# Kernel tuning notes

Measured on AMD Instinct MI355X. Metric: run time of the kernel, lower is better.

Reference implementation:

```python
import jax, jax.numpy as jnp
import numpy as np

N_NODES = 100000
N_EDGES = 1600000
NUM_GRAPHS = 1024
D_IN = 128
D_HID = 128
D_OUT = 2
LN_EPS = 1e-5


def setup_inputs() -> dict:
    key = jax.random.key(0)
    ks = jax.random.split(key, 10)
    x = jax.random.normal(ks[0], (N_NODES, D_IN), dtype=jnp.float32)
    edge_index = jax.random.randint(ks[1], (2, N_EDGES), 0, N_NODES, dtype=jnp.int64)
    batch = jnp.sort(jax.random.randint(ks[2], (N_NODES,), 0, NUM_GRAPHS, dtype=jnp.int64))
    s = 0.05  # weight scale to keep activations sane
    return {
        "x": x,
        "edge_index": edge_index,
        "batch": batch,
        "W1l": jax.random.normal(ks[3], (D_HID, D_IN), dtype=jnp.float32) * s,
        "b1l": jnp.zeros((D_HID,), dtype=jnp.float32),
        "W1r": jax.random.normal(ks[4], (D_HID, D_IN), dtype=jnp.float32) * s,
        "W2l": jax.random.normal(ks[5], (D_HID, D_HID), dtype=jnp.float32) * s,
        "b2l": jnp.zeros((D_HID,), dtype=jnp.float32),
        "W2r": jax.random.normal(ks[6], (D_HID, D_HID), dtype=jnp.float32) * s,
        "ln_g": jnp.ones((D_HID,), dtype=jnp.float32),
        "ln_b": jnp.zeros((D_HID,), dtype=jnp.float32),
        "Wlin": jax.random.normal(ks[7], (D_OUT, D_HID), dtype=jnp.float32) * s,
        "blin": jnp.zeros((D_OUT,), dtype=jnp.float32),
    }


def _sage_conv(x, src, dst, Wl, bl, Wr):
    # PyG SAGEConv with mean aggregation: lin_l(mean_{j in N(i)} x_j) + lin_r(x_i)
    msg_sum = jax.ops.segment_sum(x[src], dst, num_segments=N_NODES)
    deg = jax.ops.segment_sum(jnp.ones((src.shape[0], 1), x.dtype), dst, num_segments=N_NODES)
    agg = msg_sum / jnp.maximum(deg, 1.0)  # isolated nodes -> 0
    return agg @ Wl.T + bl + x @ Wr.T  # lin_r has no bias (PyG default)


def reference(x, edge_index, batch, W1l, b1l, W1r, W2l, b2l, W2r, ln_g, ln_b, Wlin, blin):
    src, dst = edge_index[0], edge_index[1]
    h = jax.nn.relu(_sage_conv(x, src, dst, W1l, b1l, W1r))
    h = jax.nn.relu(_sage_conv(h, src, dst, W2l, b2l, W2r))
    # global_add_pool over graphs
    g = jax.ops.segment_sum(h, batch, num_segments=NUM_GRAPHS)  # [G, D_HID]
    # LayerNorm over last dim
    mu = jnp.mean(g, axis=-1, keepdims=True)
    var = jnp.var(g, axis=-1, keepdims=True)
    gn = (g - mu) * jax.lax.rsqrt(var + LN_EPS) * ln_g + ln_b
    return gn @ Wlin.T + blin  # [G, D_OUT]
```

## Files before the change

### kernel.cpp

```cpp
#include <hip/hip_runtime.h>
#include <hip/hip_bf16.h>
#include <hip/hip_fp8.h>

#define N_NODES   100000
#define N_EDGES   1600000
#define NUM_GRAPHS 1024
#define D         128
#define LN_EPS    1e-5f
#define NBUCKETS  391
#define CAP       4864
#define CHUNK     4096

typedef __attribute__((ext_vector_type(8))) short short8;
typedef __attribute__((ext_vector_type(4))) float floatx4;
typedef __attribute__((ext_vector_type(2))) float f32x2;

static __device__ __forceinline__ float bf2f(unsigned int u) {
    return __uint_as_float(u << 16);
}
static __device__ __forceinline__ unsigned short f2bf(float f) {
    __hip_bfloat16 h = __float2bfloat16(f);
    return *reinterpret_cast<unsigned short*>(&h);
}
static __device__ __forceinline__ void acc4(f32x2* acc, uint4 v) {
    acc[0] += (f32x2){__uint_as_float(v.x << 16), __uint_as_float(v.x & 0xffff0000u)};
    acc[1] += (f32x2){__uint_as_float(v.y << 16), __uint_as_float(v.y & 0xffff0000u)};
    acc[2] += (f32x2){__uint_as_float(v.z << 16), __uint_as_float(v.z & 0xffff0000u)};
    acc[3] += (f32x2){__uint_as_float(v.w << 16), __uint_as_float(v.w & 0xffff0000u)};
}

#if __has_builtin(__builtin_amdgcn_cvt_pk_f32_fp8)
#define UNPK_FP8(x, w) __builtin_amdgcn_cvt_pk_f32_fp8((x), (w))
#else
static __device__ __forceinline__ f32x2 unpk_fp8_sw(unsigned x, bool w) {
    unsigned s = w ? (x >> 16) : (x & 0xffffu);
    __hip_fp8_e4m3 a, b;
    *reinterpret_cast<unsigned char*>(&a) = (unsigned char)(s & 0xff);
    *reinterpret_cast<unsigned char*>(&b) = (unsigned char)((s >> 8) & 0xff);
    return (f32x2){(float)a, (float)b};
}
#define UNPK_FP8(x, w) unpk_fp8_sw((x), (w))
#endif

#if __has_builtin(__builtin_amdgcn_cvt_pk_fp8_f32)
#define PK_FP8(a, b, old, w) ((unsigned)__builtin_amdgcn_cvt_pk_fp8_f32((a), (b), (int)(old), (w)))
#else
static __device__ __forceinline__ unsigned pk_fp8_sw(float a, float b) {
    __hip_fp8_e4m3 fa = (__hip_fp8_e4m3)a;
    __hip_fp8_e4m3 fb = (__hip_fp8_e4m3)b;
    return (unsigned)*reinterpret_cast<unsigned char*>(&fa) |
           ((unsigned)*reinterpret_cast<unsigned char*>(&fb) << 8);
}
#define PK_FP8(a, b, old, w) ((w) ? ((((unsigned)(old)) & 0xffffu) | (pk_fp8_sw((a),(b)) << 16)) \
                                  : ((((unsigned)(old)) & 0xffff0000u) | pk_fp8_sw((a),(b))))
#endif

__global__ __launch_bounds__(256)
void prep_kernel(const float* __restrict__ x, unsigned short* __restrict__ xbf,
                 unsigned* __restrict__ xf8,
                 const float* __restrict__ W1l, const float* __restrict__ W1r,
                 const float* __restrict__ W2l, const float* __restrict__ W2r,
                 unsigned short* __restrict__ Wc1, unsigned short* __restrict__ Wc2,
                 int* __restrict__ cursor) {
    int i = blockIdx.x * 256 + threadIdx.x;
    float4 v = reinterpret_cast<const float4*>(x)[i];
    ushort4 o;
    o.x = f2bf(v.x); o.y = f2bf(v.y); o.z = f2bf(v.z); o.w = f2bf(v.w);
    reinterpret_cast<ushort4*>(xbf)[i] = o;
    unsigned p = PK_FP8(v.x, v.y, 0u, false);
    p = PK_FP8(v.z, v.w, p, true);
    xf8[i] = p;
    if (blockIdx.x < 256) {
        int layer = i >> 15;
        int rem = i & 32767;
        int c = rem >> 8;
        int k = rem & 255;
        const float* Wl = layer ? W2l : W1l;
        const float* Wr = layer ? W2r : W1r;
        unsigned short* dst = layer ? Wc2 : Wc1;
        float wv = (k < 128) ? Wl[c * 128 + k] : Wr[c * 128 + (k - 128)];
        dst[c * 256 + k] = f2bf(wv);
    }
    if (blockIdx.x == 256) {
        for (int b = threadIdx.x; b < NBUCKETS; b += 256)
            cursor[b] = b * CAP;
    }
}

__global__ __launch_bounds__(256)
void cvt_h1_kernel(const unsigned short* __restrict__ h1, uint2* __restrict__ h1f8) {
    int i = blockIdx.x * 256 + threadIdx.x;
    uint4 v = reinterpret_cast<const uint4*>(h1)[i];
    float c0 = __uint_as_float(v.x << 16), c1 = __uint_as_float(v.x & 0xffff0000u);
    float c2 = __uint_as_float(v.y << 16), c3 = __uint_as_float(v.y & 0xffff0000u);
    float c4 = __uint_as_float(v.z << 16), c5 = __uint_as_float(v.z & 0xffff0000u);
    float c6 = __uint_as_float(v.w << 16), c7 = __uint_as_float(v.w & 0xffff0000u);
    unsigned lo = PK_FP8(c0, c1, 0u, false);
    lo = PK_FP8(c2, c3, lo, true);
    unsigned hi = PK_FP8(c4, c5, 0u, false);
    hi = PK_FP8(c6, c7, hi, true);
    h1f8[i] = make_uint2(lo, hi);
}

__global__ __launch_bounds__(256)
void bin_scatter_kernel(const int* __restrict__ src, const int* __restrict__ dst,
                        int* __restrict__ cursor, unsigned* __restrict__ binned) {
    __shared__ int cnt[NBUCKETS];
    __shared__ int base[NBUCKETS];
    int chunkBase = blockIdx.x * CHUNK;
    for (int i = threadIdx.x; i < NBUCKETS; i += 256) cnt[i] = 0;
    __syncthreads();
    int es[16], ed[16], lofs[16];
    #pragma unroll
    for (int j = 0; j < 16; ++j) {
        int e = chunkBase + j * 256 + threadIdx.x;
        if (e < N_EDGES) {
            es[j] = src[e];
            ed[j] = dst[e];
            lofs[j] = atomicAdd(&cnt[ed[j] >> 8], 1);
        }
    }
    __syncthreads();
    for (int i = threadIdx.x; i < NBUCKETS; i += 256) {
        int c = cnt[i];
        base[i] = c ? atomicAdd(&cursor[i], c) : 0;
    }
    __syncthreads();
    #pragma unroll
    for (int j = 0; j < 16; ++j) {
        int e = chunkBase + j * 256 + threadIdx.x;
        if (e < N_EDGES) {
            int b = ed[j] >> 8;
            int pos = base[b] + lofs[j];
            if (pos < (b + 1) * CAP)
                binned[pos] = ((unsigned)(ed[j] & 255) << 17) | (unsigned)es[j];
        }
    }
}

__global__ __launch_bounds__(256)
void bucket_build_kernel(const unsigned* __restrict__ binned, const int* __restrict__ cursor,
                         int2* __restrict__ row_info, int* __restrict__ src_sorted) {
    __shared__ int scnt[256];
    __shared__ int sscan[256];
    int b = blockIdx.x;
    int t = threadIdx.x;
    int lo = b * CAP;
    int hi = cursor[b];
    int cap_end = lo + CAP;
    if (hi > cap_end) hi = cap_end;
    scnt[t] = 0;
    __syncthreads();
    unsigned rec[19];
    short rnk[19];
    #pragma unroll
    for (int i = 0; i < 19; ++i) {
        int e = lo + t + i * 256;
        if (e < hi) {
            unsigned r = binned[e];
            rec[i] = r;
            rnk[i] = (short)atomicAdd(&scnt[r >> 17], 1);
        }
    }
    __syncthreads();
    int v = scnt[t];
    sscan[t] = v;
    __syncthreads();
    for (int off = 1; off < 256; off <<= 1) {
        int a = (t >= off) ? sscan[t - off] : 0;
        __syncthreads();
        sscan[t] += a;
        __syncthreads();
    }
    int ex = sscan[t] - v;
    int node = b * 256 + t;
    if (node < N_NODES) row_info[node] = make_int2(lo + ex, v);
    scnt[t] = ex;
    __syncthreads();
    #pragma unroll
    for (int i = 0; i < 19; ++i) {
        int e = lo + t + i * 256;
        if (e < hi) {
            unsigned r = rec[i];
            src_sorted[lo + scnt[r >> 17] + rnk[i]] = (int)(r & 0x1FFFFu);
        }
    }
}

__global__ __launch_bounds__(256)
void aggregate_kernel(const unsigned char* __restrict__ feat8,
                      const int* __restrict__ src_sorted,
                      const int2* __restrict__ row_info,
                      unsigned short* __restrict__ aggout) {
    int wave = threadIdx.x >> 6;
    int lane = threadIdx.x & 63;
    int node = blockIdx.x * 4 + wave;
    int sub = lane >> 4;
    int ch = (lane & 15) * 8;
    int2 ri = row_info[node];
    int s = ri.x, deg = ri.y;
    const unsigned char* fb = feat8 + ch;
    f32x2 acc[4];
    acc[0] = acc[1] = acc[2] = acc[3] = (f32x2){0.f, 0.f};

    if (deg <= 64) {
        int si = 0;
        if (lane < deg) si = src_sorted[s + lane];
        int rounds = (deg + 3) >> 2;
        for (int r = 0; r < rounds; ++r) {
            int eidx = r * 4 + sub;
            int u = __shfl(si, eidx, 64);
            if (eidx < deg) {
                uint2 v = *(const uint2*)(fb + (size_t)u * 128);
                acc[0] += UNPK_FP8(v.x, false);
                acc[1] += UNPK_FP8(v.x, true);
                acc[2] += UNPK_FP8(v.y, false);
                acc[3] += UNPK_FP8(v.y, true);
            }
        }
    } else {
        for (int j = s + sub; j < s + deg; j += 4) {
            int u = src_sorted[j];
            uint2 v = *(const uint2*)(fb + (size_t)u * 128);
            acc[0] += UNPK_FP8(v.x, false);
            acc[1] += UNPK_FP8(v.x, true);
            acc[2] += UNPK_FP8(v.y, false);
            acc[3] += UNPK_FP8(v.y, true);
        }
    }
    #pragma unroll
    for (int i = 0; i < 4; ++i) {
        acc[i].x += __shfl_xor(acc[i].x, 16, 64);
        acc[i].y += __shfl_xor(acc[i].y, 16, 64);
        acc[i].x += __shfl_xor(acc[i].x, 32, 64);
        acc[i].y += __shfl_xor(acc[i].y, 32, 64);
    }
    float inv = 1.f / (float)(deg > 1 ? deg : 1);
    if (sub == 0) {
        uint4 ov;
        ov.x = (unsigned)f2bf(acc[0].x * inv) | ((unsigned)f2bf(acc[0].y * inv) << 16);
        ov.y = (unsigned)f2bf(acc[1].x * inv) | ((unsigned)f2bf(acc[1].y * inv) << 16);
        ov.z = (unsigned)f2bf(acc[2].x * inv) | ((unsigned)f2bf(acc[2].y * inv) << 16);
        ov.w = (unsigned)f2bf(acc[3].x * inv) | ((unsigned)f2bf(acc[3].y * inv) << 16);
        *(uint4*)(aggout + (size_t)node * 128 + ch) = ov;
    }
}

__global__ __launch_bounds__(256)
void gemm_kernel(const unsigned short* __restrict__ A1,
                 const unsigned short* __restrict__ A2,
                 const unsigned short* __restrict__ Wcat,
                 const float* __restrict__ bias,
                 unsigned short* __restrict__ out) {
    __shared__ unsigned short Asm[64][32];
    __shared__ unsigned short Wsm[128][32];
    int tid = threadIdx.x;
    int wave = tid >> 6;
    int lane = tid & 63;
    int nodeBase = blockIdx.x * 64;
    floatx4 acc[4][2];
    #pragma unroll
    for (int a = 0; a < 4; ++a)
        #pragma unroll
        for (int b = 0; b < 2; ++b) acc[a][b] = (floatx4){0.f, 0.f, 0.f, 0.f};

    int r = tid >> 2, sg = tid & 3;
    int quad = lane >> 4, m = lane & 15;

    for (int kc = 0; kc < 8; ++kc) {
        const unsigned short* Asrc = (kc < 4) ? A1 : A2;
        int kOff = (kc & 3) * 32;
        int node = nodeBase + r;
        float4 av = make_float4(0.f, 0.f, 0.f, 0.f);
        if (node < N_NODES) av = *(const float4*)(Asrc + (size_t)node * 128 + kOff + sg * 8);
        *(float4*)(&Asm[r][sg * 8]) = av;
        #pragma unroll
        for (int it = 0; it < 2; ++it) {
            int idx = tid + it * 256;
            int wr = idx >> 2, wsg = idx & 3;
            *(float4*)(&Wsm[wr][wsg * 8]) = *(const float4*)(Wcat + wr * 256 + kc * 32 + wsg * 8);
        }
        __syncthreads();
        short8 afr[4], bfr[2];
        #pragma unroll
        for (int nb = 0; nb < 4; ++nb)
            afr[nb] = *(const short8*)(&Asm[nb * 16 + m][quad * 8]);
        #pragma unroll
        for (int cb = 0; cb < 2; ++cb)
            bfr[cb] = *(const short8*)(&Wsm[wave * 32 + cb * 16 + m][quad * 8]);
        #pragma unroll
        for (int nb = 0; nb < 4; ++nb)
            #pragma unroll
            for (int cb = 0; cb < 2; ++cb)
                acc[nb][cb] = __builtin_amdgcn_mfma_f32_16x16x32_bf16(afr[nb], bfr[cb], acc[nb][cb], 0, 0, 0);
        __syncthreads();
    }
    #pragma unroll
    for (int cb = 0; cb < 2; ++cb) {
        int col = wave * 32 + cb * 16 + m;
        float bv = bias[col];
        #pragma unroll
        for (int nb = 0; nb < 4; ++nb) {
            #pragma unroll
            for (int rr = 0; rr < 4; ++rr) {
                int row = nodeBase + nb * 16 + quad * 4 + rr;
                if (row < N_NODES) {
                    float v = acc[nb][cb][rr] + bv;
                    v = v > 0.f ? v : 0.f;
                    out[(size_t)row * 128 + col] = f2bf(v);
                }
            }
        }
    }
}

__global__ __launch_bounds__(256)
void pool_ln_out_kernel(const unsigned short* __restrict__ h2,
                        const int* __restrict__ batch,
                        const float* __restrict__ ln_g, const float* __restrict__ ln_b,
                        const float* __restrict__ Wlin, const float* __restrict__ blin,
                        float* __restrict__ out) {
    int g = blockIdx.x;
    int t = threadIdx.x;
    int lane = t & 63, w = t >> 6;
    __shared__ int se[2];
    if (t < 2) {
        int target = g + t;
        int lo = 0, hi = N_NODES;
        while (lo < hi) {
            int mid = (lo + hi) >> 1;
            if (batch[mid] < target) lo = mid + 1; else hi = mid;
        }
        se[t] = lo;
    }
    __syncthreads();
    int s = se[0], e = se[1];
    int ns = t >> 4;
    int chg = t & 15;
    f32x2 a[4];
    a[0] = a[1] = a[2] = a[3] = (f32x2){0.f, 0.f};
    for (int n = s + ns; n < e; n += 16) {
        uint4 v = *(const uint4*)(h2 + (size_t)n * 128 + chg * 8);
        acc4(a, v);
    }
    #pragma unroll
    for (int i = 0; i < 4; ++i) {
        a[i].x += __shfl_xor(a[i].x, 16, 64);
        a[i].y += __shfl_xor(a[i].y, 16, 64);
        a[i].x += __shfl_xor(a[i].x, 32, 64);
        a[i].y += __shfl_xor(a[i].y, 32, 64);
    }
    __shared__ float sw[4][128];
    if (lane < 16) {
        #pragma unroll
        for (int k = 0; k < 4; ++k) {
            sw[w][chg * 8 + 2 * k]     = a[k].x;
            sw[w][chg * 8 + 2 * k + 1] = a[k].y;
        }
    }
    __syncthreads();
    __shared__ float red[128];
    float sum = 0.f;
    if (t < 128) {
        sum = sw[0][t] + sw[1][t] + sw[2][t] + sw[3][t];
        red[t] = sum;
    }
    __syncthreads();
    for (int off = 64; off > 0; off >>= 1) {
        if (t < off) red[t] += red[t + off];
        __syncthreads();
    }
    float mu = red[0] * (1.f / 128.f);
    __syncthreads();
    float dv = sum - mu;
    if (t < 128) red[t] = dv * dv;
    __syncthreads();
    for (int off = 64; off > 0; off >>= 1) {
        if (t < off) red[t] += red[t + off];
        __syncthreads();
    }
    float var = red[0] * (1.f / 128.f);
    __syncthreads();
    __shared__ float r0[128], r1[128];
    if (t < 128) {
        float gn = dv * rsqrtf(var + LN_EPS) * ln_g[t] + ln_b[t];
        r0[t] = gn * Wlin[t];
        r1[t] = gn * Wlin[128 + t];
    }
    __syncthreads();
    for (int off = 64; off > 0; off >>= 1) {
        if (t < off) { r0[t] += r0[t + off]; r1[t] += r1[t + off]; }
        __syncthreads();
    }
    if (t == 0) {
        out[g * 2 + 0] = r0[0] + blin[0];
        out[g * 2 + 1] = r1[0] + blin[1];
    }
}

extern "C" void kernel_launch(void* const* d_in, const int* in_sizes, int n_in,
                              void* d_out, int out_size, void* d_ws, size_t ws_size,
                              hipStream_t stream) {
    const float* x    = (const float*)d_in[0];
    const int*   ei   = (const int*)d_in[1];
    const int*   batch= (const int*)d_in[2];
    const float* W1l  = (const float*)d_in[3];
    const float* b1l  = (const float*)d_in[4];
    const float* W1r  = (const float*)d_in[5];
    const float* W2l  = (const float*)d_in[6];
    const float* b2l  = (const float*)d_in[7];
    const float* W2r  = (const float*)d_in[8];
    const float* ln_g = (const float*)d_in[9];
    const float* ln_b = (const float*)d_in[10];
    const float* Wlin = (const float*)d_in[11];
    const float* blin = (const float*)d_in[12];
    float* out = (float*)d_out;

    char* ws = (char*)d_ws;
    size_t off = 0;
    auto alloc = [&](size_t bytes) {
        char* p = ws + off;
        off = (off + bytes + 255) & ~(size_t)255;
        return p;
    };
    unsigned short* xbf  = (unsigned short*)alloc((size_t)N_NODES * D * 2);
    unsigned short* aggb = (unsigned short*)alloc((size_t)N_NODES * D * 2);
    unsigned short* h1   = (unsigned short*)alloc((size_t)N_NODES * D * 2);
    unsigned*       xf8  = (unsigned*)alloc((size_t)N_NODES * D);
    unsigned short* Wc1  = (unsigned short*)alloc(128 * 256 * 2);
    unsigned short* Wc2  = (unsigned short*)alloc(128 * 256 * 2);
    int2* row_info   = (int2*)alloc((size_t)N_NODES * 8);
    int* src_sorted  = (int*)alloc((size_t)NBUCKETS * CAP * 4);
    int* cursor      = (int*)alloc(NBUCKETS * 4);
    unsigned* binned = (unsigned*)aggb;
    uint2* h1f8      = (uint2*)xf8;

    const int* srcI = ei;
    const int* dstI = ei + N_EDGES;

    prep_kernel<<<12500, 256, 0, stream>>>(x, xbf, xf8, W1l, W1r, W2l, W2r, Wc1, Wc2, cursor);
    bin_scatter_kernel<<<(N_EDGES + CHUNK - 1) / CHUNK, 256, 0, stream>>>(srcI, dstI, cursor, binned);
    bucket_build_kernel<<<NBUCKETS, 256, 0, stream>>>(binned, cursor, row_info, src_sorted);

    aggregate_kernel<<<25000, 256, 0, stream>>>((const unsigned char*)xf8, src_sorted, row_info, aggb);
    gemm_kernel<<<1563, 256, 0, stream>>>(aggb, xbf, Wc1, b1l, h1);
    cvt_h1_kernel<<<6250, 256, 0, stream>>>(h1, h1f8);
    aggregate_kernel<<<25000, 256, 0, stream>>>((const unsigned char*)h1f8, src_sorted, row_info, aggb);
    gemm_kernel<<<1563, 256, 0, stream>>>(aggb, h1, Wc2, b2l, xbf);
    pool_ln_out_kernel<<<NUM_GRAPHS, 256, 0, stream>>>(xbf, batch, ln_g, ln_b, Wlin, blin, out);
}
```

Baseline: 316.8 us.

## Widen aggregate gathers to 16-byte loads with LDS cross-lane reduction

```diff
diff --git a/kernel.cpp b/kernel.cpp
--- a/kernel.cpp
+++ b/kernel.cpp
@@ -54,6 +54,17 @@
 #define PK_FP8(a, b, old, w) ((w) ? ((((unsigned)(old)) & 0xffffu) | (pk_fp8_sw((a),(b)) << 16)) \
                                   : ((((unsigned)(old)) & 0xffff0000u) | pk_fp8_sw((a),(b))))
 #endif
+
+static __device__ __forceinline__ void acc_row16(f32x2* acc, uint4 v) {
+    acc[0] += UNPK_FP8(v.x, false);
+    acc[1] += UNPK_FP8(v.x, true);
+    acc[2] += UNPK_FP8(v.y, false);
+    acc[3] += UNPK_FP8(v.y, true);
+    acc[4] += UNPK_FP8(v.z, false);
+    acc[5] += UNPK_FP8(v.z, true);
+    acc[6] += UNPK_FP8(v.w, false);
+    acc[7] += UNPK_FP8(v.w, true);
+}
 
 __global__ __launch_bounds__(256)
 void prep_kernel(const float* __restrict__ x, unsigned short* __restrict__ xbf,
@@ -187,63 +198,72 @@
     }
 }
 
+#define AGG_STRIDE 140
 __global__ __launch_bounds__(256)
 void aggregate_kernel(const unsigned char* __restrict__ feat8,
                       const int* __restrict__ src_sorted,
                       const int2* __restrict__ row_info,
                       unsigned short* __restrict__ aggout) {
+    __shared__ float red[4][1120];
     int wave = threadIdx.x >> 6;
     int lane = threadIdx.x & 63;
     int node = blockIdx.x * 4 + wave;
-    int sub = lane >> 4;
-    int ch = (lane & 15) * 8;
+    int sub = lane >> 3;
+    int l8  = lane & 7;
+    unsigned chb = (unsigned)l8 * 16;
     int2 ri = row_info[node];
     int s = ri.x, deg = ri.y;
-    const unsigned char* fb = feat8 + ch;
-    f32x2 acc[4];
-    acc[0] = acc[1] = acc[2] = acc[3] = (f32x2){0.f, 0.f};
-
-    if (deg <= 64) {
+    f32x2 acc[8];
+    #pragma unroll
+    for (int i = 0; i < 8; ++i) acc[i] = (f32x2){0.f, 0.f};
+
+    for (int base = 0; base < deg; base += 64) {
+        int nb = deg - base; if (nb > 64) nb = 64;
         int si = 0;
-        if (lane < deg) si = src_sorted[s + lane];
-        int rounds = (deg + 3) >> 2;
-        for (int r = 0; r < rounds; ++r) {
-            int eidx = r * 4 + sub;
-            int u = __shfl(si, eidx, 64);
-            if (eidx < deg) {
-                uint2 v = *(const uint2*)(fb + (size_t)u * 128);
-                acc[0] += UNPK_FP8(v.x, false);
-                acc[1] += UNPK_FP8(v.x, true);
-                acc[2] += UNPK_FP8(v.y, false);
-                acc[3] += UNPK_FP8(v.y, true);
+        if (lane < nb) si = src_sorted[s + base + lane];
+        int nf = nb >> 3;
+        int r = 0;
+        for (; r + 2 <= nf; r += 2) {
+            int u0 = __shfl(si, (r << 3) + sub, 64);
+            int u1 = __shfl(si, (r << 3) + 8 + sub, 64);
+            uint4 v0 = *(const uint4*)(feat8 + (((unsigned)u0 << 7) + chb));
+            uint4 v1 = *(const uint4*)(feat8 + (((unsigned)u1 << 7) + chb));
+            acc_row16(acc, v0);
+            acc_row16(acc, v1);
+        }
+        if (r < nf) {
+            int u0 = __shfl(si, (r << 3) + sub, 64);
+            uint4 v0 = *(const uint4*)(feat8 + (((unsigned)u0 << 7) + chb));
+            acc_row16(acc, v0);
+        }
+        int tail = nb & 7;
+        if (tail) {
+            int u = __shfl(si, (nf << 3) + sub, 64);
+            if (sub < tail) {
+                uint4 v = *(const uint4*)(feat8 + (((unsigned)u << 7) + chb));
+                acc_row16(acc, v);
             }
         }
-    } else {
-        for (int j = s + sub; j < s + deg; j += 4) {
-            int u = src_sorted[j];
-            uint2 v = *(const uint2*)(fb + (size_t)u * 128);
-            acc[0] += UNPK_FP8(v.x, false);
-            acc[1] += UNPK_FP8(v.x, true);
-            acc[2] += UNPK_FP8(v.y, false);
-            acc[3] += UNPK_FP8(v.y, true);
-        }
-    }
+    }
+
+    float* wred = red[wave];
+    int wbase = sub * AGG_STRIDE + l8 * 16;
     #pragma unroll
     for (int i = 0; i < 4; ++i) {
-        acc[i].x += __shfl_xor(acc[i].x, 16, 64);
-        acc[i].y += __shfl_xor(acc[i].y, 16, 64);
-        acc[i].x += __shfl_xor(acc[i].x, 32, 64);
-        acc[i].y += __shfl_xor(acc[i].y, 32, 64);
-    }
+        floatx4 w;
+        w[0] = acc[2 * i].x;     w[1] = acc[2 * i].y;
+        w[2] = acc[2 * i + 1].x; w[3] = acc[2 * i + 1].y;
+        *(floatx4*)(&wred[wbase + 4 * i]) = w;
+    }
+    asm volatile("s_waitcnt lgkmcnt(0)" ::: "memory");
+    int rb = sub * 16 + 2 * l8;
+    f32x2 tot = (f32x2){0.f, 0.f};
+    #pragma unroll
+    for (int ss = 0; ss < 8; ++ss)
+        tot += *(const f32x2*)(&wred[ss * AGG_STRIDE + rb]);
     float inv = 1.f / (float)(deg > 1 ? deg : 1);
-    if (sub == 0) {
-        uint4 ov;
-        ov.x = (unsigned)f2bf(acc[0].x * inv) | ((unsigned)f2bf(acc[0].y * inv) << 16);
-        ov.y = (unsigned)f2bf(acc[1].x * inv) | ((unsigned)f2bf(acc[1].y * inv) << 16);
-        ov.z = (unsigned)f2bf(acc[2].x * inv) | ((unsigned)f2bf(acc[2].y * inv) << 16);
-        ov.w = (unsigned)f2bf(acc[3].x * inv) | ((unsigned)f2bf(acc[3].y * inv) << 16);
-        *(uint4*)(aggout + (size_t)node * 128 + ch) = ov;
-    }
+    unsigned o = (unsigned)f2bf(tot.x * inv) | ((unsigned)f2bf(tot.y * inv) << 16);
+    *(unsigned*)(aggout + (size_t)node * 128 + 2 * lane) = o;
 }
 
 __global__ __launch_bounds__(256)
```

New measurement: 310.3 us. -2.1%, faster.

## Fuse FP8 conversion into GEMM epilogue, register-resident weights, remap aggregate lanes

Applied to the files above, without the earlier changes.

```diff
diff --git a/kernel.cpp b/kernel.cpp
--- a/kernel.cpp
+++ b/kernel.cpp
@@ -54,6 +54,11 @@
 #define PK_FP8(a, b, old, w) ((w) ? ((((unsigned)(old)) & 0xffffu) | (pk_fp8_sw((a),(b)) << 16)) \
                                   : ((((unsigned)(old)) & 0xffff0000u) | pk_fp8_sw((a),(b))))
 #endif
+
+static __device__ __forceinline__ unsigned char fp8b(float v) {
+    __hip_fp8_e4m3 t = (__hip_fp8_e4m3)v;
+    return *reinterpret_cast<unsigned char*>(&t);
+}
 
 __global__ __launch_bounds__(256)
 void prep_kernel(const float* __restrict__ x, unsigned short* __restrict__ xbf,
@@ -84,22 +89,9 @@
     if (blockIdx.x == 256) {
         for (int b = threadIdx.x; b < NBUCKETS; b += 256)
             cursor[b] = b * CAP;
-    }
-}
-
-__global__ __launch_bounds__(256)
-void cvt_h1_kernel(const unsigned short* __restrict__ h1, uint2* __restrict__ h1f8) {
-    int i = blockIdx.x * 256 + threadIdx.x;
-    uint4 v = reinterpret_cast<const uint4*>(h1)[i];
-    float c0 = __uint_as_float(v.x << 16), c1 = __uint_as_float(v.x & 0xffff0000u);
-    float c2 = __uint_as_float(v.y << 16), c3 = __uint_as_float(v.y & 0xffff0000u);
-    float c4 = __uint_as_float(v.z << 16), c5 = __uint_as_float(v.z & 0xffff0000u);
-    float c6 = __uint_as_float(v.w << 16), c7 = __uint_as_float(v.w & 0xffff0000u);
-    unsigned lo = PK_FP8(c0, c1, 0u, false);
-    lo = PK_FP8(c2, c3, lo, true);
-    unsigned hi = PK_FP8(c4, c5, 0u, false);
-    hi = PK_FP8(c6, c7, hi, true);
-    h1f8[i] = make_uint2(lo, hi);
+        if (threadIdx.x < 32)
+            xf8[(size_t)N_NODES * 32 + threadIdx.x] = 0u;
+    }
 }
 
 __global__ __launch_bounds__(256)
@@ -192,58 +184,64 @@
                       const int* __restrict__ src_sorted,
                       const int2* __restrict__ row_info,
                       unsigned short* __restrict__ aggout) {
-    int wave = threadIdx.x >> 6;
-    int lane = threadIdx.x & 63;
-    int node = blockIdx.x * 4 + wave;
-    int sub = lane >> 4;
-    int ch = (lane & 15) * 8;
+    int tid  = threadIdx.x;
+    int wave = tid >> 6;
+    int lane = tid & 63;
+    int l16  = lane & 15;
+    int grpbase = lane & 48;
+    int node = blockIdx.x * 16 + wave * 4 + (lane >> 4);
     int2 ri = row_info[node];
     int s = ri.x, deg = ri.y;
-    const unsigned char* fb = feat8 + ch;
-    f32x2 acc[4];
-    acc[0] = acc[1] = acc[2] = acc[3] = (f32x2){0.f, 0.f};
-
-    if (deg <= 64) {
-        int si = 0;
-        if (lane < deg) si = src_sorted[s + lane];
-        int rounds = (deg + 3) >> 2;
-        for (int r = 0; r < rounds; ++r) {
-            int eidx = r * 4 + sub;
-            int u = __shfl(si, eidx, 64);
-            if (eidx < deg) {
-                uint2 v = *(const uint2*)(fb + (size_t)u * 128);
-                acc[0] += UNPK_FP8(v.x, false);
-                acc[1] += UNPK_FP8(v.x, true);
-                acc[2] += UNPK_FP8(v.y, false);
-                acc[3] += UNPK_FP8(v.y, true);
-            }
-        }
-    } else {
-        for (int j = s + sub; j < s + deg; j += 4) {
-            int u = src_sorted[j];
-            uint2 v = *(const uint2*)(fb + (size_t)u * 128);
-            acc[0] += UNPK_FP8(v.x, false);
-            acc[1] += UNPK_FP8(v.x, true);
-            acc[2] += UNPK_FP8(v.y, false);
-            acc[3] += UNPK_FP8(v.y, true);
-        }
-    }
-    #pragma unroll
-    for (int i = 0; i < 4; ++i) {
-        acc[i].x += __shfl_xor(acc[i].x, 16, 64);
-        acc[i].y += __shfl_xor(acc[i].y, 16, 64);
-        acc[i].x += __shfl_xor(acc[i].x, 32, 64);
-        acc[i].y += __shfl_xor(acc[i].y, 32, 64);
+    int dmax = deg;
+    dmax = max(dmax, __shfl_xor(dmax, 16, 64));
+    dmax = max(dmax, __shfl_xor(dmax, 32, 64));
+    unsigned chb = (unsigned)l16 * 8;
+    f32x2 a0[4], a1[4];
+    #pragma unroll
+    for (int i = 0; i < 4; ++i) { a0[i] = (f32x2){0.f, 0.f}; a1[i] = (f32x2){0.f, 0.f}; }
+
+    for (int c0 = 0; c0 < dmax; c0 += 16) {
+        int si = src_sorted[s + c0 + l16];
+        int rel = deg - c0;
+        int rend = dmax - c0; if (rend > 16) rend = 16;
+        int r = 0;
+        for (; r + 2 <= rend; r += 2) {
+            int u0 = __shfl(si, grpbase + r, 64);
+            int u1 = __shfl(si, grpbase + r + 1, 64);
+            u0 = (r < rel) ? u0 : N_NODES;
+            u1 = (r + 1 < rel) ? u1 : N_NODES;
+            uint2 v0 = *(const uint2*)(feat8 + (((unsigned)u0 << 7) + chb));
+            uint2 v1 = *(const uint2*)(feat8 + (((unsigned)u1 << 7) + chb));
+            a0[0] += UNPK_FP8(v0.x, false);
+            a0[1] += UNPK_FP8(v0.x, true);
+            a0[2] += UNPK_FP8(v0.y, false);
+            a0[3] += UNPK_FP8(v0.y, true);
+            a1[0] += UNPK_FP8(v1.x, false);
+            a1[1] += UNPK_FP8(v1.x, true);
+            a1[2] += UNPK_FP8(v1.y, false);
+            a1[3] += UNPK_FP8(v1.y, true);
+        }
+        if (r < rend) {
+            int u0 = __shfl(si, grpbase + r, 64);
+            u0 = (r < rel) ? u0 : N_NODES;
+            uint2 v0 = *(const uint2*)(feat8 + (((unsigned)u0 << 7) + chb));
+            a0[0] += UNPK_FP8(v0.x, false);
+            a0[1] += UNPK_FP8(v0.x, true);
+            a0[2] += UNPK_FP8(v0.y, false);
+            a0[3] += UNPK_FP8(v0.y, true);
+        }
     }
     float inv = 1.f / (float)(deg > 1 ? deg : 1);
-    if (sub == 0) {
-        uint4 ov;
-        ov.x = (unsigned)f2bf(acc[0].x * inv) | ((unsigned)f2bf(acc[0].y * inv) << 16);
-        ov.y = (unsigned)f2bf(acc[1].x * inv) | ((unsigned)f2bf(acc[1].y * inv) << 16);
-        ov.z = (unsigned)f2bf(acc[2].x * inv) | ((unsigned)f2bf(acc[2].y * inv) << 16);
-        ov.w = (unsigned)f2bf(acc[3].x * inv) | ((unsigned)f2bf(acc[3].y * inv) << 16);
-        *(uint4*)(aggout + (size_t)node * 128 + ch) = ov;
-    }
+    f32x2 t0 = (a0[0] + a1[0]) * inv;
+    f32x2 t1 = (a0[1] + a1[1]) * inv;
+    f32x2 t2 = (a0[2] + a1[2]) * inv;
+    f32x2 t3 = (a0[3] + a1[3]) * inv;
+    uint4 o;
+    o.x = (unsigned)f2bf(t0.x) | ((unsigned)f2bf(t0.y) << 16);
+    o.y = (unsigned)f2bf(t1.x) | ((unsigned)f2bf(t1.y) << 16);
+    o.z = (unsigned)f2bf(t2.x) | ((unsigned)f2bf(t2.y) << 16);
+    o.w = (unsigned)f2bf(t3.x) | ((unsigned)f2bf(t3.y) << 16);
+    *(uint4*)(aggout + (size_t)node * 128 + l16 * 8) = o;
 }
 
 __global__ __launch_bounds__(256)
@@ -251,50 +249,45 @@
                  const unsigned short* __restrict__ A2,
                  const unsigned short* __restrict__ Wcat,
                  const float* __restrict__ bias,
-                 unsigned short* __restrict__ out) {
-    __shared__ unsigned short Asm[64][32];
-    __shared__ unsigned short Wsm[128][32];
+                 unsigned short* __restrict__ out,
+                 unsigned char* __restrict__ f8out) {
     int tid = threadIdx.x;
     int wave = tid >> 6;
     int lane = tid & 63;
+    int quad = lane >> 4, m = lane & 15;
     int nodeBase = blockIdx.x * 64;
+
+    short8 bw[2][8];
+    #pragma unroll
+    for (int cb = 0; cb < 2; ++cb) {
+        const unsigned short* wp = Wcat + (size_t)(wave * 32 + cb * 16 + m) * 256 + quad * 8;
+        #pragma unroll
+        for (int kc = 0; kc < 8; ++kc)
+            bw[cb][kc] = *(const short8*)(wp + kc * 32);
+    }
+
     floatx4 acc[4][2];
     #pragma unroll
     for (int a = 0; a < 4; ++a)
         #pragma unroll
         for (int b = 0; b < 2; ++b) acc[a][b] = (floatx4){0.f, 0.f, 0.f, 0.f};
 
-    int r = tid >> 2, sg = tid & 3;
-    int quad = lane >> 4, m = lane & 15;
-
+    #pragma unroll
     for (int kc = 0; kc < 8; ++kc) {
         const unsigned short* Asrc = (kc < 4) ? A1 : A2;
         int kOff = (kc & 3) * 32;
-        int node = nodeBase + r;
-        float4 av = make_float4(0.f, 0.f, 0.f, 0.f);
-        if (node < N_NODES) av = *(const float4*)(Asrc + (size_t)node * 128 + kOff + sg * 8);
-        *(float4*)(&Asm[r][sg * 8]) = av;
-        #pragma unroll
-        for (int it = 0; it < 2; ++it) {
-            int idx = tid + it * 256;
-            int wr = idx >> 2, wsg = idx & 3;
-            *(float4*)(&Wsm[wr][wsg * 8]) = *(const float4*)(Wcat + wr * 256 + kc * 32 + wsg * 8);
-        }
-        __syncthreads();
-        short8 afr[4], bfr[2];
+        const unsigned short* ap = Asrc + (size_t)(nodeBase + m) * 128 + kOff + quad * 8;
+        short8 afr[4];
         #pragma unroll
         for (int nb = 0; nb < 4; ++nb)
-            afr[nb] = *(const short8*)(&Asm[nb * 16 + m][quad * 8]);
-        #pragma unroll
-        for (int cb = 0; cb < 2; ++cb)
-            bfr[cb] = *(const short8*)(&Wsm[wave * 32 + cb * 16 + m][quad * 8]);
+            afr[nb] = *(const short8*)(ap + (size_t)nb * 16 * 128);
         #pragma unroll
         for (int nb = 0; nb < 4; ++nb)
             #pragma unroll
             for (int cb = 0; cb < 2; ++cb)
-                acc[nb][cb] = __builtin_amdgcn_mfma_f32_16x16x32_bf16(afr[nb], bfr[cb], acc[nb][cb], 0, 0, 0);
-        __syncthreads();
-    }
+                acc[nb][cb] = __builtin_amdgcn_mfma_f32_16x16x32_bf16(afr[nb], bw[cb][kc], acc[nb][cb], 0, 0, 0);
+    }
+
     #pragma unroll
     for (int cb = 0; cb < 2; ++cb) {
         int col = wave * 32 + cb * 16 + m;
@@ -308,6 +301,7 @@
                     float v = acc[nb][cb][rr] + bv;
                     v = v > 0.f ? v : 0.f;
                     out[(size_t)row * 128 + col] = f2bf(v);
+                    if (f8out) f8out[(size_t)row * 128 + col] = fp8b(v);
                 }
             }
         }
@@ -426,14 +420,14 @@
     unsigned short* xbf  = (unsigned short*)alloc((size_t)N_NODES * D * 2);
     unsigned short* aggb = (unsigned short*)alloc((size_t)N_NODES * D * 2);
     unsigned short* h1   = (unsigned short*)alloc((size_t)N_NODES * D * 2);
-    unsigned*       xf8  = (unsigned*)alloc((size_t)N_NODES * D);
+    unsigned*       xf8  = (unsigned*)alloc((size_t)N_NODES * D + 128);
     unsigned short* Wc1  = (unsigned short*)alloc(128 * 256 * 2);
     unsigned short* Wc2  = (unsigned short*)alloc(128 * 256 * 2);
     int2* row_info   = (int2*)alloc((size_t)N_NODES * 8);
-    int* src_sorted  = (int*)alloc((size_t)NBUCKETS * CAP * 4);
+    int* src_sorted  = (int*)alloc(((size_t)NBUCKETS * CAP + 8192) * 4);
     int* cursor      = (int*)alloc(NBUCKETS * 4);
     unsigned* binned = (unsigned*)aggb;
-    uint2* h1f8      = (uint2*)xf8;
+    unsigned char* h1f8 = (unsigned char*)xf8;
 
     const int* srcI = ei;
     const int* dstI = ei + N_EDGES;
@@ -442,10 +436,9 @@
     bin_scatter_kernel<<<(N_EDGES + CHUNK - 1) / CHUNK, 256, 0, stream>>>(srcI, dstI, cursor, binned);
     bucket_build_kernel<<<NBUCKETS, 256, 0, stream>>>(binned, cursor, row_info, src_sorted);
 
-    aggregate_kernel<<<25000, 256, 0, stream>>>((const unsigned char*)xf8, src_sorted, row_info, aggb);
-    gemm_kernel<<<1563, 256, 0, stream>>>(aggb, xbf, Wc1, b1l, h1);
-    cvt_h1_kernel<<<6250, 256, 0, stream>>>(h1, h1f8);
-    aggregate_kernel<<<25000, 256, 0, stream>>>((const unsigned char*)h1f8, src_sorted, row_info, aggb);
-    gemm_kernel<<<1563, 256, 0, stream>>>(aggb, h1, Wc2, b2l, xbf);
+    aggregate_kernel<<<6250, 256, 0, stream>>>((const unsigned char*)xf8, src_sorted, row_info, aggb);
+    gemm_kernel<<<1563, 256, 0, stream>>>(aggb, xbf, Wc1, b1l, h1, h1f8);
+    aggregate_kernel<<<6250, 256, 0, stream>>>(h1f8, src_sorted, row_info, aggb);
+    gemm_kernel<<<1563, 256, 0, stream>>>(aggb, h1, Wc2, b2l, xbf, nullptr);
     pool_ln_out_kernel<<<NUM_GRAPHS, 256, 0, stream>>>(xbf, batch, ln_g, ln_b, Wlin, blin, out);
 }
```

Measured after the change: 335.0 us. 1.06x slower.
